# Performance work log

Hardware: AMD Instinct MI355X
Metric: run time of the kernel (lower is better)

## Reference

```python
import jax, jax.numpy as jnp
import numpy as np


def _ternary(x, delta):
    # {-1, 0, +1} thresholded at +/- delta
    return jnp.where(x > delta, 1.0, jnp.where(x < -delta, -1.0, 0.0)).astype(x.dtype)


def setup_inputs() -> dict:
    key = jax.random.key(0)
    kx, kw = jax.random.split(key)
    x = jax.random.normal(kx, (8192, 4096), dtype=jnp.float32)
    weight = jax.random.normal(kw, (4096, 4096), dtype=jnp.float32) * 0.02
    return {"x": x, "weight": weight}


def reference(x, weight):
    # TernaryActivation: delta = 0.1 * mean|x|
    x_q = _ternary(x, 0.1 * jnp.mean(jnp.abs(x)))
    # TernaryQuantize: delta = 0.05 * mean|w|, scaled by alpha = mean|w|
    w_abs_mean = jnp.mean(jnp.abs(weight))
    w_q = w_abs_mean * _ternary(weight, 0.05 * w_abs_mean)
    # F.linear(x_q, w_q) = x_q @ w_q.T
    return jnp.einsum('bi,oi->bo', x_q, w_q)
```

## Files before the change

kernel.cpp:

```cpp
#include <hip/hip_runtime.h>
#include <stdint.h>

typedef __attribute__((ext_vector_type(4))) int i32x4;
typedef __attribute__((ext_vector_type(16))) float f32x16;

#define MROWS 8192L
#define NCOLS 4096L
#define KDIM  4096L

#define XQ_BYTES   (MROWS * KDIM / 2)
#define WQ_BYTES   (NCOLS * KDIM / 2)
#define SCAL_OFF   (XQ_BYTES + WQ_BYTES)

__global__ __launch_bounds__(256) void k_reduce_abs(const float* __restrict__ x,
                                                    const float* __restrict__ w,
                                                    float* __restrict__ partials) {
    __shared__ float sm[256];
    int b = blockIdx.x;
    int t = threadIdx.x;
    const float4* v;
    long base;
    if (b < 512) { v = (const float4*)x; base = (long)b * 16384; }
    else         { v = (const float4*)w; base = (long)(b - 512) * 16384; }
    float s = 0.f;
    for (int i = t; i < 16384; i += 256) {
        float4 q = v[base + i];
        s += fabsf(q.x) + fabsf(q.y) + fabsf(q.z) + fabsf(q.w);
    }
    sm[t] = s;
    __syncthreads();
    for (int off = 128; off > 0; off >>= 1) {
        if (t < off) sm[t] += sm[t + off];
        __syncthreads();
    }
    if (t == 0) partials[b] = sm[0];
}

__global__ __launch_bounds__(256) void k_finalize(float* __restrict__ scal) {
    const float* partials = scal + 4;
    __shared__ double sm[256];
    int t = threadIdx.x;

    double sx = 0.0;
    for (int i = t; i < 512; i += 256) sx += (double)partials[i];
    sm[t] = sx;
    __syncthreads();
    for (int off = 128; off > 0; off >>= 1) {
        if (t < off) sm[t] += sm[t + off];
        __syncthreads();
    }
    double SX = sm[0];
    __syncthreads();

    double sw = (double)partials[512 + t];
    sm[t] = sw;
    __syncthreads();
    for (int off = 128; off > 0; off >>= 1) {
        if (t < off) sm[t] += sm[t + off];
        __syncthreads();
    }
    if (t == 0) {
        float meanx = (float)(SX / 33554432.0);
        float meanw = (float)(sm[0] / 16777216.0);
        scal[0] = 0.1f * meanx;
        scal[1] = 0.05f * meanw;
        scal[2] = meanw;
    }
}

__device__ __forceinline__ unsigned int nib4(float v, float delta) {
    return v > delta ? 2u : (v < -delta ? 10u : 0u);
}

__global__ __launch_bounds__(256) void k_quant4(const float* __restrict__ x,
                                                const float* __restrict__ w,
                                                unsigned int* __restrict__ xq,
                                                unsigned int* __restrict__ wq,
                                                const float* __restrict__ scal) {
    int b = blockIdx.x;
    const float* src;
    unsigned int* dst;
    float delta;
    long i0, stride, total8;
    if (b < 2048) {
        src = x; dst = xq; delta = scal[0];
        i0 = (long)b * 256 + threadIdx.x; stride = 2048L * 256; total8 = MROWS * KDIM / 8;
    } else {
        src = w; dst = wq; delta = scal[1];
        i0 = (long)(b - 2048) * 256 + threadIdx.x; stride = 1024L * 256; total8 = NCOLS * KDIM / 8;
    }
    const float4* s4 = (const float4*)src;
    for (long i = i0; i < total8; i += stride) {
        float4 q0 = s4[2 * i];
        float4 q1 = s4[2 * i + 1];
        unsigned int wd = nib4(q0.x, delta)
                        | (nib4(q0.y, delta) << 4)
                        | (nib4(q0.z, delta) << 8)
                        | (nib4(q0.w, delta) << 12)
                        | (nib4(q1.x, delta) << 16)
                        | (nib4(q1.y, delta) << 20)
                        | (nib4(q1.z, delta) << 24)
                        | (nib4(q1.w, delta) << 28);
        dst[i] = wd;
    }
}

#define GLOAD_LDS16(g, l)                                                             \
    __builtin_amdgcn_global_load_lds((const __attribute__((address_space(1))) void*)(g), \
                                     (__attribute__((address_space(3))) void*)(l),       \
                                     16, 0, 0)

#define MK8(v) __builtin_shufflevector((v), (v), 0, 1, 2, 3, -1, -1, -1, -1)

#define MFMA32(a, b, c)                                                       \
    __builtin_amdgcn_mfma_scale_f32_32x32x64_f8f6f4(MK8(a), MK8(b), (c),      \
        4, 4, 0, 0x7F7F7F7F, 0, 0x7F7F7F7F)

__global__ __launch_bounds__(512, 2) void k_gemm(const signed char* __restrict__ Xq,
                                                 const signed char* __restrict__ Wq,
                                                 float* __restrict__ out,
                                                 const float* __restrict__ scal) {
    __shared__ __attribute__((aligned(16))) signed char lds[131072];

    const float alpha = scal[2];

    int bid = (int)blockIdx.x;
    bid = (bid & 7) * 64 + (bid >> 3);
    int bm = bid >> 4;
    int bn = bid & 15;
    long row0 = (long)bm * 256;
    long col0 = (long)bn * 256;

    int t = threadIdx.x;
    int lane = t & 63;
    int wid = t >> 6;
    int wm = wid >> 2;
    int wn = wid & 3;

    const signed char* sp[4];
    int ldoff[4];
#pragma unroll
    for (int j = 0; j < 4; ++j) {
        int g = wid * 4 + j;
        ldoff[j] = g * 1024;
        if (g < 16) {
            long grow = row0 + (g >> 3) * 128 + ((g >> 1) & 3) * 32 + (lane & 31);
            sp[j] = Xq + grow * 2048 + (g & 1) * 32 + (lane >> 5) * 16;
        } else {
            int h = g - 16;
            long grow = col0 + (h >> 2) * 64 + ((h >> 1) & 1) * 32 + (lane & 31);
            sp[j] = Wq + grow * 2048 + (h & 1) * 32 + (lane >> 5) * 16;
        }
    }

#define STAGE(slot, g1) do {                                                   \
    signed char* sb_ = lds + (slot) * 32768;                                   \
    _Pragma("unroll")                                                          \
    for (int j_ = 0; j_ < 4; ++j_)                                             \
        GLOAD_LDS16(sp[j_] + (long)(g1) * 64, sb_ + ldoff[j_]);                \
} while (0)

    const signed char* Ab = lds + wm * 8192 + lane * 16;
    const signed char* Bb = lds + 16384 + wn * 4096 + lane * 16;

    f32x16 acc[4][2];
#pragma unroll
    for (int i = 0; i < 4; ++i)
#pragma unroll
        for (int j = 0; j < 2; ++j)
            acc[i][j] = (f32x16){0.f};

    STAGE(0, 0);
    STAGE(1, 1);
    STAGE(2, 2);

    for (int g = 0; g < 32; ++g) {
        int slot = g & 3;
        __builtin_amdgcn_s_barrier();
        if (g < 29) {
            STAGE((g + 3) & 3, g + 3);
            asm volatile("s_waitcnt vmcnt(12)" ::: "memory");
        } else if (g == 29) {
            asm volatile("s_waitcnt vmcnt(8)" ::: "memory");
        } else if (g == 30) {
            asm volatile("s_waitcnt vmcnt(4)" ::: "memory");
        } else {
            asm volatile("s_waitcnt vmcnt(0)" ::: "memory");
        }
        __builtin_amdgcn_s_barrier();
        __builtin_amdgcn_sched_barrier(0);

        const signed char* A = Ab + slot * 32768;
        const signed char* B = Bb + slot * 32768;

        i32x4 a00, a01, a10, a11, a20, a21, a30, a31;
        i32x4 b00, b01, b10, b11;
        b00 = *(const i32x4*)(B + 0 * 1024);
        b01 = *(const i32x4*)(B + 1 * 1024);
        b10 = *(const i32x4*)(B + 2 * 1024);
        b11 = *(const i32x4*)(B + 3 * 1024);
        a00 = *(const i32x4*)(A + 0 * 1024);
        a01 = *(const i32x4*)(A + 1 * 1024);
        a10 = *(const i32x4*)(A + 2 * 1024);
        a11 = *(const i32x4*)(A + 3 * 1024);
        __builtin_amdgcn_s_setprio(1);
        acc[0][0] = MFMA32(a00, b00, acc[0][0]);
        acc[0][1] = MFMA32(a00, b10, acc[0][1]);
        acc[1][0] = MFMA32(a10, b00, acc[1][0]);
        acc[1][1] = MFMA32(a10, b10, acc[1][1]);
        acc[0][0] = MFMA32(a01, b01, acc[0][0]);
        acc[0][1] = MFMA32(a01, b11, acc[0][1]);
        acc[1][0] = MFMA32(a11, b01, acc[1][0]);
        acc[1][1] = MFMA32(a11, b11, acc[1][1]);
        __builtin_amdgcn_s_setprio(0);
        a20 = *(const i32x4*)(A + 4 * 1024);
        a21 = *(const i32x4*)(A + 5 * 1024);
        a30 = *(const i32x4*)(A + 6 * 1024);
        a31 = *(const i32x4*)(A + 7 * 1024);
        __builtin_amdgcn_s_setprio(1);
        acc[2][0] = MFMA32(a20, b00, acc[2][0]);
        acc[2][1] = MFMA32(a20, b10, acc[2][1]);
        acc[3][0] = MFMA32(a30, b00, acc[3][0]);
        acc[3][1] = MFMA32(a30, b10, acc[3][1]);
        acc[2][0] = MFMA32(a21, b01, acc[2][0]);
        acc[2][1] = MFMA32(a21, b11, acc[2][1]);
        acc[3][0] = MFMA32(a31, b01, acc[3][0]);
        acc[3][1] = MFMA32(a31, b11, acc[3][1]);
        __builtin_amdgcn_s_setprio(0);
    }

#pragma unroll
    for (int mi = 0; mi < 4; ++mi) {
#pragma unroll
        for (int ni = 0; ni < 2; ++ni) {
            long col = col0 + wn * 64 + ni * 32 + (lane & 31);
            long rowb = row0 + wm * 128 + mi * 32 + 4 * (lane >> 5);
#pragma unroll
            for (int r = 0; r < 16; ++r) {
                long row = rowb + (r & 3) + 8 * (r >> 2);
                out[row * NCOLS + col] = alpha * acc[mi][ni][r];
            }
        }
    }
#undef STAGE
}

extern "C" void kernel_launch(void* const* d_in, const int* in_sizes, int n_in,
                              void* d_out, int out_size, void* d_ws, size_t ws_size,
                              hipStream_t stream) {
    const float* x = (const float*)d_in[0];
    const float* w = (const float*)d_in[1];
    float* out = (float*)d_out;

    uint8_t* ws = (uint8_t*)d_ws;
    signed char* Xq = (signed char*)ws;
    signed char* Wq = (signed char*)(ws + XQ_BYTES);
    float* scal = (float*)(ws + SCAL_OFF);

    k_reduce_abs<<<768, 256, 0, stream>>>(x, w, scal + 4);
    k_finalize<<<1, 256, 0, stream>>>(scal);
    k_quant4<<<3072, 256, 0, stream>>>(x, w, (unsigned int*)Xq, (unsigned int*)Wq, scal);
    k_gemm<<<512, 512, 0, stream>>>(Xq, Wq, out, scal);
}
```

Before: 179.4 us.

## Pre-tile quantized FP4 operands into MFMA-fragment order for contiguous GEMM staging

The quantize kernel now writes FP4 data in a blocked layout: each 32-row by 128-K chunk is stored as contiguous 1 KB fragments matching the lanes' MFMA operand order. The GEMM's global-to-LDS loads then read one contiguous 1 KB span per wave per stage instead of 32 rows strided by 2 KB. This should improve load coalescing and DRAM/L2 efficiency in the GEMM. In exchange, the quantize kernel's reads become strided (each lane reads 128 bytes from its own row) and it writes 16 bytes per lane.

```diff
diff --git a/kernel.cpp b/kernel.cpp
--- a/kernel.cpp
+++ b/kernel.cpp
@@ -72,37 +72,46 @@
     return v > delta ? 2u : (v < -delta ? 10u : 0u);
 }
 
-__global__ __launch_bounds__(256) void k_quant4(const float* __restrict__ x,
+__global__ __launch_bounds__(256) void k_quantF(const float* __restrict__ x,
                                                 const float* __restrict__ w,
-                                                unsigned int* __restrict__ xq,
-                                                unsigned int* __restrict__ wq,
+                                                uint4* __restrict__ xq,
+                                                uint4* __restrict__ wq,
                                                 const float* __restrict__ scal) {
-    int b = blockIdx.x;
+    int wv = blockIdx.x * 4 + (threadIdx.x >> 6);
+    int l = threadIdx.x & 63;
+
     const float* src;
-    unsigned int* dst;
+    uint4* dst;
     float delta;
-    long i0, stride, total8;
-    if (b < 2048) {
-        src = x; dst = xq; delta = scal[0];
-        i0 = (long)b * 256 + threadIdx.x; stride = 2048L * 256; total8 = MROWS * KDIM / 8;
+    int task;
+    if (wv < 16384) {
+        src = x; dst = xq; delta = scal[0]; task = wv;
     } else {
-        src = w; dst = wq; delta = scal[1];
-        i0 = (long)(b - 2048) * 256 + threadIdx.x; stride = 1024L * 256; total8 = NCOLS * KDIM / 8;
-    }
-    const float4* s4 = (const float4*)src;
-    for (long i = i0; i < total8; i += stride) {
-        float4 q0 = s4[2 * i];
-        float4 q1 = s4[2 * i + 1];
-        unsigned int wd = nib4(q0.x, delta)
-                        | (nib4(q0.y, delta) << 4)
-                        | (nib4(q0.z, delta) << 8)
-                        | (nib4(q0.w, delta) << 12)
-                        | (nib4(q1.x, delta) << 16)
-                        | (nib4(q1.y, delta) << 20)
-                        | (nib4(q1.z, delta) << 24)
-                        | (nib4(q1.w, delta) << 28);
-        dst[i] = wd;
-    }
+        src = w; dst = wq; delta = scal[1]; task = wv - 16384;
+    }
+    int rowblk = task >> 6;
+    int rest = task & 63;
+    long row = (long)rowblk * 32 + (l & 31);
+    long fidx = row * 4096 + (long)(rest >> 1) * 128 + (long)(rest & 1) * 64
+              + (long)(l >> 5) * 32;
+    const float4* s4 = (const float4*)(src + fidx);
+
+    unsigned int ow[4];
+#pragma unroll
+    for (int c = 0; c < 4; ++c) {
+        float4 q0 = s4[2 * c];
+        float4 q1 = s4[2 * c + 1];
+        ow[c] = nib4(q0.x, delta)
+              | (nib4(q0.y, delta) << 4)
+              | (nib4(q0.z, delta) << 8)
+              | (nib4(q0.w, delta) << 12)
+              | (nib4(q1.x, delta) << 16)
+              | (nib4(q1.y, delta) << 20)
+              | (nib4(q1.z, delta) << 24)
+              | (nib4(q1.w, delta) << 28);
+    }
+    uint4 o; o.x = ow[0]; o.y = ow[1]; o.z = ow[2]; o.w = ow[3];
+    dst[(long)task * 64 + l] = o;
 }
 
 #define GLOAD_LDS16(g, l)                                                             \
@@ -144,12 +153,12 @@
         int g = wid * 4 + j;
         ldoff[j] = g * 1024;
         if (g < 16) {
-            long grow = row0 + (g >> 3) * 128 + ((g >> 1) & 3) * 32 + (lane & 31);
-            sp[j] = Xq + grow * 2048 + (g & 1) * 32 + (lane >> 5) * 16;
+            long rowblk = bm * 8 + (g >> 3) * 4 + ((g >> 1) & 3);
+            sp[j] = Xq + rowblk * 65536 + (g & 1) * 1024 + lane * 16;
         } else {
             int h = g - 16;
-            long grow = col0 + (h >> 2) * 64 + ((h >> 1) & 1) * 32 + (lane & 31);
-            sp[j] = Wq + grow * 2048 + (h & 1) * 32 + (lane >> 5) * 16;
+            long colblk = bn * 8 + (h >> 2) * 2 + ((h >> 1) & 1);
+            sp[j] = Wq + colblk * 65536 + (h & 1) * 1024 + lane * 16;
         }
     }
 
@@ -157,7 +166,7 @@
     signed char* sb_ = lds + (slot) * 32768;                                   \
     _Pragma("unroll")                                                          \
     for (int j_ = 0; j_ < 4; ++j_)                                             \
-        GLOAD_LDS16(sp[j_] + (long)(g1) * 64, sb_ + ldoff[j_]);                \
+        GLOAD_LDS16(sp[j_] + (long)(g1) * 2048, sb_ + ldoff[j_]);              \
 } while (0)
 
     const signed char* Ab = lds + wm * 8192 + lane * 16;
@@ -259,6 +268,6 @@
 
     k_reduce_abs<<<768, 256, 0, stream>>>(x, w, scal + 4);
     k_finalize<<<1, 256, 0, stream>>>(scal);
-    k_quant4<<<3072, 256, 0, stream>>>(x, w, (unsigned int*)Xq, (unsigned int*)Wq, scal);
+    k_quantF<<<6144, 256, 0, stream>>>(x, w, (uint4*)Xq, (uint4*)Wq, scal);
     k_gemm<<<512, 512, 0, stream>>>(Xq, Wq, out, scal);
 }
```

Result: faster. 156.3 us (-12.9%).
